# Kernel optimization log

Measured on AMD Instinct MI355X. Metric: run time of the kernel, lower is better.

Reference implementation:

```python
import jax, jax.numpy as jnp
import numpy as np

# MORR all-pass ring parameters (MORRConfig_20um defaults: attenuation / self-coupling)
A_MORR = 0.8578
R_MORR = 0.8578
KS = 3       # kernel_size
MB = 8       # miniblock (circulant block size)
BN_EPS = 1e-5


def mrr_roundtrip_phase_to_tr(phi):
    # through-port transmission of an all-pass microring vs roundtrip phase
    c = jnp.cos(phi)
    num = A_MORR * A_MORR - 2.0 * A_MORR * R_MORR * c + R_MORR * R_MORR
    den = 1.0 - 2.0 * A_MORR * R_MORR * c + (A_MORR * R_MORR) ** 2
    return num / den


def setup_inputs() -> dict:
    key = jax.random.key(0)
    k1, k2 = jax.random.split(key, 2)
    B, C, H, W = 64, 64, 32, 32
    outC = 64
    q = (C * KS * KS + MB - 1) // MB   # grid_dim_x = 72
    p = (outC + MB - 1) // MB          # grid_dim_y = 8
    x = jax.random.normal(k1, (B, C, H, W), jnp.float32)
    weight = jax.random.normal(k2, (p, q, MB), jnp.float32) * 0.05  # circulant eigen-vectors per block
    gamma = jnp.ones((outC,), jnp.float32)   # BatchNorm2d weight
    beta = jnp.zeros((outC,), jnp.float32)   # BatchNorm2d bias
    return {"x": x, "weight": weight, "gamma": gamma, "beta": beta}


def reference(x, weight, gamma, beta):
    B, C, H, W = x.shape
    p, q, mb = weight.shape
    outC = gamma.shape[0]
    Ho, Wo = H, W  # stride=1, padding=1, ks=3
    L = Ho * Wo
    # im2col (torch F.unfold ordering: C major, then kh, kw)
    xp = jnp.pad(x, ((0, 0), (0, 0), (1, 1), (1, 1)))
    cols = jnp.stack([xp[:, :, i:i + Ho, j:j + Wo]
                      for i in range(KS) for j in range(KS)], axis=2)  # [B,C,9,Ho,Wo]
    cols = cols.reshape(B, C * KS * KS, L).transpose(0, 2, 1)          # [B,L,C*k*k]
    assert C * KS * KS == q * mb, "patch dim must pad to q*mb"
    s = cols.reshape(B, L, q, mb)
    s = s * s  # optical intensity (power) fed into the MORR
    # block-circulant weight: Wc[p,q,i,j] = weight[p,q,(i-j) mod mb]
    i_idx = jnp.arange(mb)
    idx = (i_idx[:, None] - i_idx[None, :]) % mb
    Wc = weight[:, :, idx]                                             # [p,q,mb,mb]
    # accumulated roundtrip phase per output node
    phase = jnp.einsum('blqj,pqij->blpi', s, Wc)                       # [B,L,p,mb]
    tr = mrr_roundtrip_phase_to_tr(phase)
    out = tr.reshape(B, L, p * mb)[:, :, :outC]                        # truncate to out_channel
    out = out.transpose(0, 2, 1).reshape(B, outC, Ho, Wo)
    # BatchNorm2d (training mode: batch statistics) + Hardtanh(-1, 1)
    mean = out.mean(axis=(0, 2, 3), keepdims=True)
    var = out.var(axis=(0, 2, 3), keepdims=True)
    y = (out - mean) * jax.lax.rsqrt(var + BN_EPS)
    y = y * gamma[None, :, None, None] + beta[None, :, None, None]
    return jnp.clip(y, -1.0, 1.0)
```

## Files before the change

### kernel.cpp

```cpp
#include <hip/hip_runtime.h>


#define A_MORR 0.8578f
#define R_MORR 0.8578f
#define TR_C1 (A_MORR * A_MORR + R_MORR * R_MORR)
#define TR_C2 (-2.0f * A_MORR * R_MORR)
#define TR_C3 (1.0f + (A_MORR * R_MORR) * (A_MORR * R_MORR))
#define BN_EPS 1e-5f

#define NPIX 65536
#define X2_LO 26112
#define SMEM_BYTES 52224
#define NBLK 512

typedef __attribute__((ext_vector_type(8))) short bf16x8;
typedef __attribute__((ext_vector_type(16))) float f32x16;

__device__ __forceinline__ void bf16split(float s, unsigned short& h, unsigned short& l) {
    union { float f; unsigned u; } cv; cv.f = s;
    unsigned r = (cv.u + 0x7fffu + ((cv.u >> 16) & 1u)) & 0xffff0000u;
    h = (unsigned short)(r >> 16);
    union { unsigned u; float f; } hv; hv.u = r;
    float lo = s - hv.f;
    cv.f = lo;
    unsigned r2 = cv.u + 0x7fffu + ((cv.u >> 16) & 1u);
    l = (unsigned short)(r2 >> 16);
}

__global__ __launch_bounds__(256) void prep_kernel(const float* __restrict__ w,
                                                   char* __restrict__ wfrag) {
    int gtid = blockIdx.x * 256 + threadIdx.x;
    if (gtid < 36864) {
        int j    = gtid & 7;
        int lane = (gtid >> 3) & 63;
        int okm  = gtid >> 9;
        int mt   = okm & 1;
        int ks   = (okm >> 1) & 3;
        int off  = okm >> 3;
        int oc   = mt * 32 + (lane & 31);
        int c    = ks * 16 + (lane >> 5) * 8 + j;
        int kg   = c * 9 + off;
        float val = w[(oc >> 3) * 576 + (kg >> 3) * 8 + ((oc - kg) & 7)];
        unsigned short h, l;
        bf16split(val, h, l);
        ((unsigned short*)(wfrag + okm * 2048))[lane * 8 + j] = h;
        ((unsigned short*)(wfrag + okm * 2048 + 1024))[lane * 8 + j] = l;
    }
}

__global__ __launch_bounds__(512, 2) void conv_kernel(const float* __restrict__ x,
                                                      const char* __restrict__ wfrag,
                                                      float* __restrict__ out,
                                                      float* __restrict__ partials) {
    const int rt  = blockIdx.x;
    const int b   = blockIdx.y;
    const int bid = b * 8 + rt;
    const int tid = threadIdx.x;

    const int lane = tid & 63;
    const int wv   = tid >> 6;
    const int wmt  = wv & 1;
    const int kq   = wv >> 1;
    const int col  = lane & 31;
    const int hs   = lane >> 5;

    __shared__ __align__(16) char smem[SMEM_BYTES];

    bf16x8 wh[9], wl[9];
    {
        const char* wbase = wfrag + (size_t)wmt * 2048 + kq * 4096 + lane * 16;
#pragma unroll
        for (int t = 0; t < 9; ++t) {
            wh[t] = *(const bf16x8*)(wbase + t * 16384);
            wl[t] = *(const bf16x8*)(wbase + t * 16384 + 1024);
        }
    }

    if (tid < 192) {
        int prec = tid & 1;
        int g    = (tid >> 1) & 7;
        int rc   = tid >> 4;
        int r    = rc >> 1;
        int c    = (rc & 1) ? 33 : 0;
        *(uint4*)(smem + prec * X2_LO + ((r * 34 + c) << 7) + (g << 4)) = uint4{0, 0, 0, 0};
    }

    {
        const int rh  = tid & 1;
        const int co  = (tid >> 1) & 7;
        const int chp = tid >> 4;
        const float* xb = x + (size_t)(b * 64 + 2 * chp) * 1024;
#pragma unroll
        for (int r3 = 0; r3 < 3; ++r3) {
            int rr = rh * 3 + r3;
            int gr = rt * 4 - 1 + rr;
            float4 a0 = {0.f, 0.f, 0.f, 0.f}, a1 = {0.f, 0.f, 0.f, 0.f};
            if (gr >= 0 && gr < 32) {
                const float* rp = xb + gr * 32 + co * 4;
                a0 = *(const float4*)rp;
                a1 = *(const float4*)(rp + 1024);
            }
            float s0[4] = {a0.x * a0.x, a0.y * a0.y, a0.z * a0.z, a0.w * a0.w};
            float s1[4] = {a1.x * a1.x, a1.y * a1.y, a1.z * a1.z, a1.w * a1.w};
#pragma unroll
            for (int i = 0; i < 4; ++i) {
                unsigned short h0, l0, h1, l1;
                bf16split(s0[i], h0, l0);
                bf16split(s1[i], h1, l1);
                int c    = 1 + co * 4 + i;
                int base = ((rr * 34 + c) << 7) + (((chp >> 2) ^ (c & 7)) << 4)
                         + ((chp & 3) << 2);
                *(unsigned*)(smem + base)         = (unsigned)h0 | ((unsigned)h1 << 16);
                *(unsigned*)(smem + X2_LO + base) = (unsigned)l0 | ((unsigned)l1 << 16);
            }
        }
    }
    __syncthreads();

    f32x16 acc0, acc1, acc2, acc3;
#pragma unroll
    for (int i = 0; i < 16; ++i) { acc0[i] = 0.f; acc1[i] = 0.f; acc2[i] = 0.f; acc3[i] = 0.f; }

#pragma unroll
    for (int dj = 0; dj < 3; ++dj) {
        const int c  = col + dj;
        const int g  = (((kq * 2 + hs) ^ (c & 7)) << 4);
        bf16x8 bh[6], bl[6];
#pragma unroll
        for (int rr = 0; rr < 6; ++rr) {
            const char* sp = smem + ((rr * 34 + c) << 7) + g;
            bh[rr] = *(const bf16x8*)sp;
            bl[rr] = *(const bf16x8*)(sp + X2_LO);
        }
#pragma unroll
        for (int di = 0; di < 3; ++di) {
            const bf16x8 ah = wh[di * 3 + dj];
            const bf16x8 al = wl[di * 3 + dj];
            acc0 = __builtin_amdgcn_mfma_f32_32x32x16_bf16(ah, bh[di + 0], acc0, 0, 0, 0);
            acc1 = __builtin_amdgcn_mfma_f32_32x32x16_bf16(ah, bh[di + 1], acc1, 0, 0, 0);
            acc2 = __builtin_amdgcn_mfma_f32_32x32x16_bf16(ah, bh[di + 2], acc2, 0, 0, 0);
            acc3 = __builtin_amdgcn_mfma_f32_32x32x16_bf16(ah, bh[di + 3], acc3, 0, 0, 0);
            acc0 = __builtin_amdgcn_mfma_f32_32x32x16_bf16(ah, bl[di + 0], acc0, 0, 0, 0);
            acc1 = __builtin_amdgcn_mfma_f32_32x32x16_bf16(ah, bl[di + 1], acc1, 0, 0, 0);
            acc2 = __builtin_amdgcn_mfma_f32_32x32x16_bf16(ah, bl[di + 2], acc2, 0, 0, 0);
            acc3 = __builtin_amdgcn_mfma_f32_32x32x16_bf16(ah, bl[di + 3], acc3, 0, 0, 0);
            acc0 = __builtin_amdgcn_mfma_f32_32x32x16_bf16(al, bh[di + 0], acc0, 0, 0, 0);
            acc1 = __builtin_amdgcn_mfma_f32_32x32x16_bf16(al, bh[di + 1], acc1, 0, 0, 0);
            acc2 = __builtin_amdgcn_mfma_f32_32x32x16_bf16(al, bh[di + 2], acc2, 0, 0, 0);
            acc3 = __builtin_amdgcn_mfma_f32_32x32x16_bf16(al, bh[di + 3], acc3, 0, 0, 0);
        }
    }

    float* mg = (float*)smem;
#define SLOT_W() do {                                                          \
    _Pragma("unroll") for (int j = 0; j < 16; ++j) {                           \
        mg[((wmt * 4 + 0) * 16 + j) * 64 + lane] = acc0[j];                    \
        mg[((wmt * 4 + 1) * 16 + j) * 64 + lane] = acc1[j];                    \
        mg[((wmt * 4 + 2) * 16 + j) * 64 + lane] = acc2[j];                    \
        mg[((wmt * 4 + 3) * 16 + j) * 64 + lane] = acc3[j];                    \
    } } while (0)
#define SLOT_A() do {                                                          \
    _Pragma("unroll") for (int j = 0; j < 16; ++j) {                           \
        acc0[j] += mg[((wmt * 4 + 0) * 16 + j) * 64 + lane];                   \
        acc1[j] += mg[((wmt * 4 + 1) * 16 + j) * 64 + lane];                   \
        acc2[j] += mg[((wmt * 4 + 2) * 16 + j) * 64 + lane];                   \
        acc3[j] += mg[((wmt * 4 + 3) * 16 + j) * 64 + lane];                   \
    } } while (0)

    __syncthreads();
    if (kq == 3) SLOT_W();
    __syncthreads();
    if (kq == 1) SLOT_A();
    __syncthreads();
    if (kq == 2) SLOT_W();
    __syncthreads();
    if (kq == 0) SLOT_A();
    __syncthreads();
    if (kq == 1) SLOT_W();
    __syncthreads();

    float* red1 = (float*)(smem + 32768);
    float* red2 = red1 + 64 * 33;

    if (kq == 0) {
        SLOT_A();
        float ts1[16], ts2[16];
#pragma unroll
        for (int j = 0; j < 16; ++j) { ts1[j] = 0.f; ts2[j] = 0.f; }
        const size_t obase = ((size_t)b * 64 + wmt * 32) * 1024 + rt * 128;
#define ROW_EPI(R, ACC) do {                                                   \
    _Pragma("unroll") for (int j = 0; j < 16; ++j) {                           \
        float cp = __cosf(ACC[j]);                                             \
        float t  = fmaf(TR_C2, cp, TR_C1) / fmaf(TR_C2, cp, TR_C3);            \
        int ocl  = (j & 3) + 8 * (j >> 2) + 4 * hs;                            \
        out[obase + (size_t)ocl * 1024 + (R) * 32 + col] = t;                  \
        ts1[j] += t; ts2[j] += t * t;                                          \
    } } while (0)
        ROW_EPI(0, acc0);
        ROW_EPI(1, acc1);
        ROW_EPI(2, acc2);
        ROW_EPI(3, acc3);
#pragma unroll
        for (int j = 0; j < 16; ++j) {
            int ocl = (j & 3) + 8 * (j >> 2) + 4 * hs;
            red1[(wmt * 32 + ocl) * 33 + col] = ts1[j];
            red2[(wmt * 32 + ocl) * 33 + col] = ts2[j];
        }
    }
    __syncthreads();
    if (tid < 64) {
        float s1 = 0.f, s2 = 0.f;
#pragma unroll
        for (int q = 0; q < 32; ++q) {
            s1 += red1[tid * 33 + q];
            s2 += red2[tid * 33 + q];
        }
        partials[(size_t)tid * NBLK + bid]        = s1;
        partials[(size_t)(64 + tid) * NBLK + bid] = s2;
    }
}

__global__ __launch_bounds__(512) void stats_kernel(const float* __restrict__ partials,
                                                    const float* __restrict__ gamma,
                                                    const float* __restrict__ beta,
                                                    float* __restrict__ ss) {
    const int c   = blockIdx.x;
    const int tid = threadIdx.x;
    __shared__ float r1[512], r2[512];
    r1[tid] = partials[(size_t)c * NBLK + tid];
    r2[tid] = partials[(size_t)(64 + c) * NBLK + tid];
    __syncthreads();
#pragma unroll
    for (int s = 256; s > 0; s >>= 1) {
        if (tid < s) {
            r1[tid] += r1[tid + s];
            r2[tid] += r2[tid + s];
        }
        __syncthreads();
    }
    if (tid == 0) {
        const float invN = 1.0f / (float)NPIX;
        float mean = r1[0] * invN;
        float var  = r2[0] * invN - mean * mean;
        float sc   = gamma[c] * rsqrtf(var + BN_EPS);
        ss[c]      = sc;
        ss[64 + c] = beta[c] - mean * sc;
    }
}

__global__ __launch_bounds__(256) void norm_kernel(float* __restrict__ out,
                                                   const float* __restrict__ ss) {
    int i = blockIdx.x * 256 + threadIdx.x;
    float4 v = ((float4*)out)[i];
    int oc = (i >> 8) & 63;
    float sc = ss[oc];
    float sh = ss[64 + oc];
    v.x = fminf(1.0f, fmaxf(-1.0f, fmaf(v.x, sc, sh)));
    v.y = fminf(1.0f, fmaxf(-1.0f, fmaf(v.y, sc, sh)));
    v.z = fminf(1.0f, fmaxf(-1.0f, fmaf(v.z, sc, sh)));
    v.w = fminf(1.0f, fmaxf(-1.0f, fmaf(v.w, sc, sh)));
    ((float4*)out)[i] = v;
}

extern "C" void kernel_launch(void* const* d_in, const int* in_sizes, int n_in,
                              void* d_out, int out_size, void* d_ws, size_t ws_size,
                              hipStream_t stream) {
    const float* x     = (const float*)d_in[0];
    const float* w     = (const float*)d_in[1];
    const float* gamma = (const float*)d_in[2];
    const float* beta  = (const float*)d_in[3];
    float* out = (float*)d_out;

    char*  wfrag    = (char*)d_ws;
    float* partials = (float*)((char*)d_ws + 147456);
    float* ss       = partials + 128 * NBLK;

    hipLaunchKernelGGL(prep_kernel, dim3(144), dim3(256), 0, stream, w, wfrag);
    hipLaunchKernelGGL(conv_kernel, dim3(8, 64), dim3(512), 0, stream, x, wfrag, out, partials);
    hipLaunchKernelGGL(stats_kernel, dim3(64), dim3(512), 0, stream, partials, gamma, beta, ss);
    hipLaunchKernelGGL(norm_kernel, dim3(4096), dim3(256), 0, stream, out, ss);
}
```

Before: 45.91 us.

## Process two row tiles per block with double-buffered LDS staging

Each conv block now handles two consecutive row tiles instead of one, which halves the grid. The weight fragments are loaded into registers once and reused for both tiles. The second tile's global loads are issued before the first tile's MFMA loop, and its LDS write happens afterwards into a second buffer, so the load latency overlaps with compute. Dynamic shared memory doubles to about 102 KB per block, which can lower occupancy (two blocks per CU would need about 204 KB) and leaves only 256 blocks to spread across the CUs.

```diff
diff --git a/kernel.cpp b/kernel.cpp
--- a/kernel.cpp
+++ b/kernel.cpp
@@ -10,7 +10,8 @@
 
 #define NPIX 65536
 #define X2_LO 26112
-#define SMEM_BYTES 52224
+#define BUF_BYTES 52224
+#define SMEM_TOTAL 104448
 #define NBLK 512
 
 typedef __attribute__((ext_vector_type(8))) short bf16x8;
@@ -48,87 +49,85 @@
     }
 }
 
-__global__ __launch_bounds__(512, 2) void conv_kernel(const float* __restrict__ x,
-                                                      const char* __restrict__ wfrag,
-                                                      float* __restrict__ out,
-                                                      float* __restrict__ partials) {
-    const int rt  = blockIdx.x;
-    const int b   = blockIdx.y;
-    const int bid = b * 8 + rt;
-    const int tid = threadIdx.x;
-
-    const int lane = tid & 63;
-    const int wv   = tid >> 6;
-    const int wmt  = wv & 1;
-    const int kq   = wv >> 1;
-    const int col  = lane & 31;
-    const int hs   = lane >> 5;
-
-    __shared__ __align__(16) char smem[SMEM_BYTES];
-
-    bf16x8 wh[9], wl[9];
-    {
-        const char* wbase = wfrag + (size_t)wmt * 2048 + kq * 4096 + lane * 16;
-#pragma unroll
-        for (int t = 0; t < 9; ++t) {
-            wh[t] = *(const bf16x8*)(wbase + t * 16384);
-            wl[t] = *(const bf16x8*)(wbase + t * 16384 + 1024);
-        }
-    }
-
+__device__ __forceinline__ void halo_zero(char* buf, int tid) {
     if (tid < 192) {
         int prec = tid & 1;
         int g    = (tid >> 1) & 7;
         int rc   = tid >> 4;
         int r    = rc >> 1;
         int c    = (rc & 1) ? 33 : 0;
-        *(uint4*)(smem + prec * X2_LO + ((r * 34 + c) << 7) + (g << 4)) = uint4{0, 0, 0, 0};
-    }
-
-    {
-        const int rh  = tid & 1;
-        const int co  = (tid >> 1) & 7;
-        const int chp = tid >> 4;
-        const float* xb = x + (size_t)(b * 64 + 2 * chp) * 1024;
-#pragma unroll
-        for (int r3 = 0; r3 < 3; ++r3) {
-            int rr = rh * 3 + r3;
-            int gr = rt * 4 - 1 + rr;
-            float4 a0 = {0.f, 0.f, 0.f, 0.f}, a1 = {0.f, 0.f, 0.f, 0.f};
-            if (gr >= 0 && gr < 32) {
-                const float* rp = xb + gr * 32 + co * 4;
-                a0 = *(const float4*)rp;
-                a1 = *(const float4*)(rp + 1024);
-            }
-            float s0[4] = {a0.x * a0.x, a0.y * a0.y, a0.z * a0.z, a0.w * a0.w};
-            float s1[4] = {a1.x * a1.x, a1.y * a1.y, a1.z * a1.z, a1.w * a1.w};
-#pragma unroll
-            for (int i = 0; i < 4; ++i) {
-                unsigned short h0, l0, h1, l1;
-                bf16split(s0[i], h0, l0);
-                bf16split(s1[i], h1, l1);
-                int c    = 1 + co * 4 + i;
-                int base = ((rr * 34 + c) << 7) + (((chp >> 2) ^ (c & 7)) << 4)
-                         + ((chp & 3) << 2);
-                *(unsigned*)(smem + base)         = (unsigned)h0 | ((unsigned)h1 << 16);
-                *(unsigned*)(smem + X2_LO + base) = (unsigned)l0 | ((unsigned)l1 << 16);
-            }
-        }
-    }
-    __syncthreads();
-
-    f32x16 acc0, acc1, acc2, acc3;
-#pragma unroll
-    for (int i = 0; i < 16; ++i) { acc0[i] = 0.f; acc1[i] = 0.f; acc2[i] = 0.f; acc3[i] = 0.f; }
-
+        *(uint4*)(buf + prec * X2_LO + ((r * 34 + c) << 7) + (g << 4)) = uint4{0, 0, 0, 0};
+    }
+}
+
+__device__ __forceinline__ void stage_load(float4 (&pre)[3][2], const float* __restrict__ x,
+                                           int rt, int b, int tid) {
+    const int rh  = tid & 1;
+    const int co  = (tid >> 1) & 7;
+    const int chp = tid >> 4;
+    const float* xb = x + (size_t)(b * 64 + 2 * chp) * 1024;
+#pragma unroll
+    for (int r3 = 0; r3 < 3; ++r3) {
+        int rr = rh * 3 + r3;
+        int gr = rt * 4 - 1 + rr;
+        float4 a0 = {0.f, 0.f, 0.f, 0.f}, a1 = {0.f, 0.f, 0.f, 0.f};
+        if (gr >= 0 && gr < 32) {
+            const float* rp = xb + gr * 32 + co * 4;
+            a0 = *(const float4*)rp;
+            a1 = *(const float4*)(rp + 1024);
+        }
+        pre[r3][0] = a0;
+        pre[r3][1] = a1;
+    }
+}
+
+__device__ __forceinline__ void stage_write(char* buf, const float4 (&pre)[3][2], int tid) {
+    const int rh  = tid & 1;
+    const int co  = (tid >> 1) & 7;
+    const int chp = tid >> 4;
+#pragma unroll
+    for (int r3 = 0; r3 < 3; ++r3) {
+        int rr = rh * 3 + r3;
+        const float4 a0 = pre[r3][0];
+        const float4 a1 = pre[r3][1];
+        float s0[4] = {a0.x * a0.x, a0.y * a0.y, a0.z * a0.z, a0.w * a0.w};
+        float s1[4] = {a1.x * a1.x, a1.y * a1.y, a1.z * a1.z, a1.w * a1.w};
+#pragma unroll
+        for (int i = 0; i < 4; ++i) {
+            unsigned short h0, l0, h1, l1;
+            bf16split(s0[i], h0, l0);
+            bf16split(s1[i], h1, l1);
+            int c    = 1 + co * 4 + i;
+            int base = ((rr * 34 + c) << 7) + (((chp >> 2) ^ (c & 7)) << 4)
+                     + ((chp & 3) << 2);
+            *(unsigned*)(buf + base)         = (unsigned)h0 | ((unsigned)h1 << 16);
+            *(unsigned*)(buf + X2_LO + base) = (unsigned)l0 | ((unsigned)l1 << 16);
+        }
+    }
+}
+
+__device__ __forceinline__ void preload_w(const char* __restrict__ wfrag,
+                                          int wmt, int kq, int lane,
+                                          bf16x8* wh, bf16x8* wl) {
+    const char* wbase = wfrag + (size_t)wmt * 2048 + kq * 4096 + lane * 16;
+#pragma unroll
+    for (int t = 0; t < 9; ++t) {
+        wh[t] = *(const bf16x8*)(wbase + t * 16384);
+        wl[t] = *(const bf16x8*)(wbase + t * 16384 + 1024);
+    }
+}
+
+__device__ __forceinline__ void kloop(const char* buf, const bf16x8* wh, const bf16x8* wl,
+                                      int kq, int hs, int col,
+                                      f32x16& acc0, f32x16& acc1, f32x16& acc2, f32x16& acc3) {
 #pragma unroll
     for (int dj = 0; dj < 3; ++dj) {
-        const int c  = col + dj;
-        const int g  = (((kq * 2 + hs) ^ (c & 7)) << 4);
+        const int c = col + dj;
+        const int g = (((kq * 2 + hs) ^ (c & 7)) << 4);
         bf16x8 bh[6], bl[6];
 #pragma unroll
         for (int rr = 0; rr < 6; ++rr) {
-            const char* sp = smem + ((rr * 34 + c) << 7) + g;
+            const char* sp = buf + ((rr * 34 + c) << 7) + g;
             bh[rr] = *(const bf16x8*)sp;
             bl[rr] = *(const bf16x8*)(sp + X2_LO);
         }
@@ -150,8 +149,14 @@
             acc3 = __builtin_amdgcn_mfma_f32_32x32x16_bf16(al, bh[di + 3], acc3, 0, 0, 0);
         }
     }
-
-    float* mg = (float*)smem;
+}
+
+__device__ __forceinline__ void merge_epi(char* scratch, float* __restrict__ out,
+                                          float* __restrict__ partials,
+                                          int bid, int b, int rt, int tid,
+                                          int lane, int wmt, int kq, int col, int hs,
+                                          f32x16& acc0, f32x16& acc1, f32x16& acc2, f32x16& acc3) {
+    float* mg = (float*)scratch;
 #define SLOT_W() do {                                                          \
     _Pragma("unroll") for (int j = 0; j < 16; ++j) {                           \
         mg[((wmt * 4 + 0) * 16 + j) * 64 + lane] = acc0[j];                    \
@@ -179,7 +184,7 @@
     if (kq == 1) SLOT_W();
     __syncthreads();
 
-    float* red1 = (float*)(smem + 32768);
+    float* red1 = (float*)(scratch + 32768);
     float* red2 = red1 + 64 * 33;
 
     if (kq == 0) {
@@ -206,6 +211,7 @@
             red1[(wmt * 32 + ocl) * 33 + col] = ts1[j];
             red2[(wmt * 32 + ocl) * 33 + col] = ts2[j];
         }
+#undef ROW_EPI
     }
     __syncthreads();
     if (tid < 64) {
@@ -218,6 +224,63 @@
         partials[(size_t)tid * NBLK + bid]        = s1;
         partials[(size_t)(64 + tid) * NBLK + bid] = s2;
     }
+#undef SLOT_W
+#undef SLOT_A
+}
+
+__global__ __launch_bounds__(512, 2) void conv_kernel(const float* __restrict__ x,
+                                                      const char* __restrict__ wfrag,
+                                                      float* __restrict__ out,
+                                                      float* __restrict__ partials) {
+    extern __shared__ __align__(16) char smem[];
+    char* buf0 = smem;
+    char* buf1 = smem + BUF_BYTES;
+
+    const int bx  = blockIdx.x;
+    const int b   = blockIdx.y;
+    const int rt0 = 2 * bx;
+    const int rt1 = 2 * bx + 1;
+    const int tid = threadIdx.x;
+
+    const int lane = tid & 63;
+    const int wv   = tid >> 6;
+    const int wmt  = wv & 1;
+    const int kq   = wv >> 1;
+    const int col  = lane & 31;
+    const int hs   = lane >> 5;
+
+    bf16x8 wh[9], wl[9];
+    preload_w(wfrag, wmt, kq, lane, wh, wl);
+
+    halo_zero(buf0, tid);
+    halo_zero(buf1, tid);
+
+    {
+        float4 p0[3][2];
+        stage_load(p0, x, rt0, b, tid);
+        stage_write(buf0, p0, tid);
+    }
+    __syncthreads();
+
+    f32x16 acc0, acc1, acc2, acc3;
+#pragma unroll
+    for (int i = 0; i < 16; ++i) { acc0[i] = 0.f; acc1[i] = 0.f; acc2[i] = 0.f; acc3[i] = 0.f; }
+
+    float4 p1[3][2];
+    stage_load(p1, x, rt1, b, tid);
+    kloop(buf0, wh, wl, kq, hs, col, acc0, acc1, acc2, acc3);
+    stage_write(buf1, p1, tid);
+    __syncthreads();
+
+    merge_epi(buf0, out, partials, b * 8 + rt0, b, rt0, tid,
+              lane, wmt, kq, col, hs, acc0, acc1, acc2, acc3);
+
+#pragma unroll
+    for (int i = 0; i < 16; ++i) { acc0[i] = 0.f; acc1[i] = 0.f; acc2[i] = 0.f; acc3[i] = 0.f; }
+    kloop(buf1, wh, wl, kq, hs, col, acc0, acc1, acc2, acc3);
+
+    merge_epi(buf0, out, partials, b * 8 + rt1, b, rt1, tid,
+              lane, wmt, kq, col, hs, acc0, acc1, acc2, acc3);
 }
 
 __global__ __launch_bounds__(512) void stats_kernel(const float* __restrict__ partials,
@@ -276,7 +339,8 @@
     float* ss       = partials + 128 * NBLK;
 
     hipLaunchKernelGGL(prep_kernel, dim3(144), dim3(256), 0, stream, w, wfrag);
-    hipLaunchKernelGGL(conv_kernel, dim3(8, 64), dim3(512), 0, stream, x, wfrag, out, partials);
+    hipLaunchKernelGGL(conv_kernel, dim3(4, 64), dim3(512), SMEM_TOTAL, stream,
+                       x, wfrag, out, partials);
     hipLaunchKernelGGL(stats_kernel, dim3(64), dim3(512), 0, stream, partials, gamma, beta, ss);
     hipLaunchKernelGGL(norm_kernel, dim3(4096), dim3(256), 0, stream, out, ss);
 }
```

Result: faster. 44.45 us (-3.2%).
